# Kernel optimization log

Hardware: AMD Instinct MI355X
Metric: run time of the kernel (lower is better)

The kernel has to match this reference:

```python
import jax, jax.numpy as jnp
import numpy as np

L = 128          # lifted_dim
NS = 50000       # source nodes
NT = 50000       # target nodes
E = 640000       # edges
SLOPE = 0.01     # cfg.leaky_slope (torch LeakyReLU default)
EPS = 1e-5       # BatchNorm eps


def _glorot(key, shape):
    fan_in, fan_out = shape[0], shape[1]
    lim = np.sqrt(6.0 / (fan_in + fan_out)).astype(np.float32)
    return jax.random.uniform(key, shape, jnp.float32, -lim, lim)


def setup_inputs() -> dict:
    key = jax.random.key(0)
    ks = jax.random.split(key, 16)
    x_s = jax.random.normal(ks[0], (NS, L), jnp.float32)
    x_t = jax.random.normal(ks[1], (NT, L), jnp.float32)
    edge_index = jax.random.randint(ks[2], (2, E), 0, NT, jnp.int64)
    edge_attr = jax.random.normal(ks[3], (E, L), jnp.float32)
    x_u = jax.random.normal(ks[4], (L,), jnp.float32)
    M = 2 * L  # message_dim
    U = 4 * L  # update_dim
    params = {
        'W1': _glorot(ks[5], (M, M)), 'b1': jnp.zeros((M,), jnp.float32),
        'W2': _glorot(ks[6], (M, M)), 'b2': jnp.zeros((M,), jnp.float32),
        'U1': _glorot(ks[7], (U, U)), 'c1': jnp.zeros((U,), jnp.float32),
        'U2': _glorot(ks[8], (U, L)), 'c2': jnp.zeros((L,), jnp.float32),
        'gamma': jnp.ones((L,), jnp.float32), 'beta': jnp.zeros((L,), jnp.float32),
    }
    return dict(x_s=x_s, x_t=x_t, edge_index=edge_index, edge_attr=edge_attr, x_u=x_u, **params)


def reference(x_s, x_t, edge_index, edge_attr, x_u,
              W1, b1, W2, b2, U1, c1, U2, c2, gamma, beta):
    src, tgt = edge_index[0], edge_index[1]
    # edge messages: gather source features + edge attrs -> 2-layer MLP
    msg = jnp.concatenate([x_s[src], edge_attr], axis=1)          # [E, 2L]
    msg = jax.nn.leaky_relu(msg @ W1 + b1, negative_slope=SLOPE)
    msg = msg @ W2 + b2                                           # [E, 2L]
    # scatter-add aggregation onto target nodes
    agg = jax.ops.segment_sum(msg, tgt, num_segments=x_t.shape[0])  # [NT, 2L]
    # node update
    xu = jnp.broadcast_to(x_u[None, :], (x_t.shape[0], x_u.shape[0]))
    h = jnp.concatenate([x_t, agg, xu], axis=-1)                  # [NT, 4L]
    h = jax.nn.leaky_relu(h @ U1 + c1, negative_slope=SLOPE)
    h = h @ U2 + c2                                               # [NT, L]
    # BatchNorm1d (training mode: batch statistics, biased variance)
    mu = jnp.mean(h, axis=0)
    var = jnp.var(h, axis=0)
    return gamma * (h - mu) * jax.lax.rsqrt(var + EPS) + beta
```

## Files before the change

kernel.cpp:

```cpp
#include <hip/hip_runtime.h>

typedef unsigned int u32;
typedef unsigned short u16;
typedef __attribute__((ext_vector_type(8))) short short8;
typedef __attribute__((ext_vector_type(8))) unsigned short ushort8v;
typedef __attribute__((ext_vector_type(4))) unsigned short ushort4v;
typedef __attribute__((ext_vector_type(4))) float f32x4;

#define NSRC 50000
#define NTGT 50000
#define NEDGE 640000
#define LDIM 128
#define SLOPE 0.01f

#define MFMA(a, b, c) __builtin_amdgcn_mfma_f32_16x16x32_bf16((a), (b), (c), 0, 0, 0)

__device__ __forceinline__ u16 f2bf(float f) {
  union { float f; u32 u; } v; v.f = f;
  u32 r = v.u + 0x7FFFu + ((v.u >> 16) & 1u);
  return (u16)(r >> 16);
}
__device__ __forceinline__ float bf2f(u16 h) {
  union { u32 u; float f; } v; v.u = ((u32)h) << 16; return v.f;
}

__global__ void k_w2b(const float* __restrict__ W2, const float* __restrict__ U1,
                      float* __restrict__ w2b) {
  const int i = blockIdx.x;
  const int j = threadIdx.x;
  const float* __restrict__ u = U1 + (size_t)128 * 512;
  float a0 = 0.f, a1 = 0.f;
#pragma unroll 8
  for (int k = 0; k < 256; ++k) {
    float w = W2[(size_t)i * 256 + k];
    a0 += w * u[(size_t)k * 512 + j];
    a1 += w * u[(size_t)k * 512 + j + 256];
  }
  w2b[(size_t)i * 512 + j] = a0;
  w2b[(size_t)i * 512 + j + 256] = a1;
}

__global__ void k_bias(const float* __restrict__ U1, const float* __restrict__ xu,
                       const float* __restrict__ b2, const float* __restrict__ c1,
                       float* __restrict__ c1e, float* __restrict__ vb) {
  const int j = threadIdx.x;
  float s = c1[j];
#pragma unroll 4
  for (int k = 0; k < 128; ++k) s += xu[k] * U1[(size_t)(384 + k) * 512 + j];
  float v = 0.f;
#pragma unroll 4
  for (int k = 0; k < 256; ++k) v += b2[k] * U1[(size_t)(128 + k) * 512 + j];
  c1e[j] = s;
  vb[j] = v;
}

__global__ void k_prep(const float* __restrict__ W1, const float* __restrict__ U1,
                       const float* __restrict__ U2, const float* __restrict__ w2b,
                       u16* __restrict__ w1a, u16* __restrict__ w1b,
                       u16* __restrict__ u1e, u16* __restrict__ u2p) {
  int id = blockIdx.x * 256 + threadIdx.x;
  int lane = id & 63, quad = (lane >> 4), l16 = lane & 15;
  if (id < 4096) {
    int g = id >> 6;
    int kc = g >> 4, cb = g & 15;
    const float* s = W1 + (size_t)(kc * 32 + quad * 8) * 256 + cb * 16 + l16;
    ushort8v p;
#pragma unroll
    for (int j = 0; j < 8; ++j) p[j] = f2bf(s[(size_t)j * 256]);
    *(ushort8v*)(w1a + ((size_t)g * 64 + lane) * 8) = p;
  } else if (id < 8192) {
    int g = (id - 4096) >> 6;
    int kc = g >> 4, cb = g & 15;
    const float* s = W1 + (size_t)(128 + kc * 32 + quad * 8) * 256 + cb * 16 + l16;
    ushort8v p;
#pragma unroll
    for (int j = 0; j < 8; ++j) p[j] = f2bf(s[(size_t)j * 256]);
    *(ushort8v*)(w1b + ((size_t)g * 64 + lane) * 8) = p;
  } else if (id < 32768) {
    int g = (id - 8192) >> 6;
    int kc = g >> 5, cb = g & 31;
    int col = cb * 16 + l16;
    ushort8v p;
#pragma unroll
    for (int j = 0; j < 8; ++j) {
      int row = kc * 32 + quad * 8 + j;
      float v = (row < 128) ? U1[(size_t)row * 512 + col]
                            : w2b[(size_t)(row - 128) * 512 + col];
      p[j] = f2bf(v);
    }
    *(ushort8v*)(u1e + ((size_t)g * 64 + lane) * 8) = p;
  } else if (id < 40960) {
    int g = (id - 32768) >> 6;
    int kc = g >> 3, cb = g & 7;
    const float* s = U2 + (size_t)(kc * 32 + quad * 8) * 128 + cb * 16 + l16;
    ushort8v p;
#pragma unroll
    for (int j = 0; j < 8; ++j) p[j] = f2bf(s[(size_t)j * 128]);
    *(ushort8v*)(u2p + ((size_t)g * 64 + lane) * 8) = p;
  }
}

__global__ void k_count(const int* __restrict__ tgt, int* __restrict__ cnt,
                        int* __restrict__ rank) {
  int e = blockIdx.x * 256 + threadIdx.x;
  if (e < NEDGE) rank[e] = atomicAdd(&cnt[tgt[e]], 1);
}

__global__ void k_scan(const int* __restrict__ cnt, int* __restrict__ rowstart) {
  __shared__ int part[1024];
  int tid = threadIdx.x;
  int base = tid * 49;
  int s = 0;
  for (int i = 0; i < 49; ++i) { int idx = base + i; if (idx < NTGT) s += cnt[idx]; }
  part[tid] = s;
  __syncthreads();
  for (int off = 1; off < 1024; off <<= 1) {
    int v = (tid >= off) ? part[tid - off] : 0;
    __syncthreads();
    part[tid] += v;
    __syncthreads();
  }
  int run = (tid > 0) ? part[tid - 1] : 0;
  for (int i = 0; i < 49; ++i) {
    int idx = base + i;
    if (idx < NTGT) { rowstart[idx] = run; run += cnt[idx]; }
  }
  if (tid == 1023) rowstart[NTGT] = part[1023];
}

__global__ void k_pos(const int* __restrict__ tgt, const int* __restrict__ rowstart,
                      int* __restrict__ pos) {
  int e = blockIdx.x * 256 + threadIdx.x;
  if (e < NEDGE) pos[e] = rowstart[tgt[e]] + pos[e];
}

__global__ void k_inv(const int* __restrict__ pos, int* __restrict__ order) {
  int e = blockIdx.x * 256 + threadIdx.x;
  if (e < NEDGE) order[pos[e]] = e;
}

__global__ __launch_bounds__(256, 3) void k_pgemm(
    const float* __restrict__ xs, const u16* __restrict__ w1ap,
    const float* __restrict__ b1, u16* __restrict__ P) {
  __shared__ u16 At[64][136];
  __shared__ u16 Ot[64][264];
  const int tid = threadIdx.x;
  const int base = blockIdx.x * 64;
  {
    const int et = tid >> 2, p = tid & 3;
    const int row = base + et;
    u16* dst = &At[et][p * 32];
    if (row < NSRC) {
      const float4* f4 = (const float4*)(xs + (size_t)row * LDIM + p * 32);
#pragma unroll
      for (int i = 0; i < 4; ++i) {
        float4 a = f4[2 * i], b = f4[2 * i + 1];
        ushort8v pk = { f2bf(a.x), f2bf(a.y), f2bf(a.z), f2bf(a.w),
                        f2bf(b.x), f2bf(b.y), f2bf(b.z), f2bf(b.w) };
        *(ushort8v*)(dst + i * 8) = pk;
      }
    } else {
      ushort8v z = {0, 0, 0, 0, 0, 0, 0, 0};
#pragma unroll
      for (int i = 0; i < 4; ++i) *(ushort8v*)(dst + i * 8) = z;
    }
  }
  __syncthreads();

  const int lane = tid & 63, wid = tid >> 6;
  const int quad = lane >> 4, l16 = lane & 15;
  const int colb = wid * 64;
  const short8* __restrict__ wf = (const short8*)w1ap;

  f32x4 acc[4][4];
#pragma unroll
  for (int a = 0; a < 4; ++a)
#pragma unroll
    for (int b = 0; b < 4; ++b) acc[a][b] = (f32x4){0.f, 0.f, 0.f, 0.f};
#pragma unroll
  for (int kc = 0; kc < 4; ++kc) {
    short8 af[4], bfr[4];
#pragma unroll
    for (int ct = 0; ct < 4; ++ct)
      bfr[ct] = wf[(size_t)(kc * 16 + wid * 4 + ct) * 64 + lane];
#pragma unroll
    for (int rt = 0; rt < 4; ++rt)
      af[rt] = *(const short8*)&At[rt * 16 + l16][kc * 32 + quad * 8];
#pragma unroll
    for (int rt = 0; rt < 4; ++rt)
#pragma unroll
      for (int ct = 0; ct < 4; ++ct)
        acc[rt][ct] = MFMA(af[rt], bfr[ct], acc[rt][ct]);
  }
#pragma unroll
  for (int ct = 0; ct < 4; ++ct) {
    int col = colb + ct * 16 + l16;
    float bias = b1[col];
#pragma unroll
    for (int rt = 0; rt < 4; ++rt)
#pragma unroll
      for (int r = 0; r < 4; ++r) {
        int row = rt * 16 + quad * 4 + r;
        Ot[row][col] = f2bf(acc[rt][ct][r] + bias);
      }
  }
  __syncthreads();
  {
    const int et = tid >> 2, p = tid & 3;
    const int row = base + et;
    if (row < NSRC) {
      u16* dst = P + (size_t)row * 256 + p * 64;
      const u16* sl = &Ot[et][p * 64];
#pragma unroll
      for (int i = 0; i < 8; ++i)
        *(ushort8v*)(dst + i * 8) = *(const ushort8v*)(sl + i * 8);
    }
  }
}

__global__ __launch_bounds__(256, 3) void k_edge(
    const float* __restrict__ ea, const int* __restrict__ srcp,
    const int* __restrict__ tgtp, const int* __restrict__ order,
    const u16* __restrict__ Pg, const u16* __restrict__ w1bp,
    float* __restrict__ agg) {
  __shared__ u16 At[64][136];
  __shared__ u16 Pt[64][264];
  __shared__ int s_tgt[64];
  const int tid = threadIdx.x;
  const int base = blockIdx.x * 64;

  {
    const int et = tid >> 2, p = tid & 3;
    const int e = order[base + et];
    if (p == 0) s_tgt[et] = tgtp[e];
    if (p < 2) {
      const float4* f4 = (const float4*)(ea + (size_t)e * LDIM + p * 64);
      u16* dst = &At[et][p * 64];
#pragma unroll
      for (int i = 0; i < 8; ++i) {
        float4 a = f4[2 * i], b = f4[2 * i + 1];
        ushort8v pk = { f2bf(a.x), f2bf(a.y), f2bf(a.z), f2bf(a.w),
                        f2bf(b.x), f2bf(b.y), f2bf(b.z), f2bf(b.w) };
        *(ushort8v*)(dst + i * 8) = pk;
      }
    } else {
      int sidx = srcp[e];
      const ushort8v* pr = (const ushort8v*)(Pg + (size_t)sidx * 256 + (p - 2) * 128);
      u16* dst = &Pt[et][(p - 2) * 128];
#pragma unroll
      for (int i = 0; i < 16; ++i) *(ushort8v*)(dst + i * 8) = pr[i];
    }
  }
  __syncthreads();

  const int lane = tid & 63, wid = tid >> 6;
  const int quad = lane >> 4, l16 = lane & 15;
  const int colb = wid * 64;
  const short8* __restrict__ wf = (const short8*)w1bp;

  f32x4 acc[4][4];
#pragma unroll
  for (int a = 0; a < 4; ++a)
#pragma unroll
    for (int b = 0; b < 4; ++b) acc[a][b] = (f32x4){0.f, 0.f, 0.f, 0.f};
#pragma unroll
  for (int kc = 0; kc < 4; ++kc) {
    short8 af[4], bfr[4];
#pragma unroll
    for (int ct = 0; ct < 4; ++ct)
      bfr[ct] = wf[(size_t)(kc * 16 + wid * 4 + ct) * 64 + lane];
#pragma unroll
    for (int rt = 0; rt < 4; ++rt)
      af[rt] = *(const short8*)&At[rt * 16 + l16][kc * 32 + quad * 8];
#pragma unroll
    for (int rt = 0; rt < 4; ++rt)
#pragma unroll
      for (int ct = 0; ct < 4; ++ct)
        acc[rt][ct] = MFMA(af[rt], bfr[ct], acc[rt][ct]);
  }
#pragma unroll
  for (int ct = 0; ct < 4; ++ct) {
    int col = colb + ct * 16 + l16;
#pragma unroll
    for (int rt = 0; rt < 4; ++rt)
#pragma unroll
      for (int r = 0; r < 4; ++r) {
        int row = rt * 16 + quad * 4 + r;
        float v = acc[rt][ct][r] + bf2f(Pt[row][col]);
        v = v > 0.f ? v : SLOPE * v;
        Pt[row][col] = f2bf(v);
      }
  }
  __syncthreads();

  {
    const int col = tid;
    float accv = 0.f;
    int prev = s_tgt[0];
    int segstart = 0;
    for (int r = 0; r < 64; ++r) {
      int t = s_tgt[r];
      if (t != prev) {
        float* dst = agg + (size_t)prev * 256 + col;
        if (segstart == 0) atomicAdd(dst, accv);
        else *dst = accv;
        accv = 0.f; prev = t; segstart = r;
      }
      accv += bf2f(Pt[r][col]);
    }
    atomicAdd(agg + (size_t)prev * 256 + col, accv);
  }
}

__global__ __launch_bounds__(256, 4) void k_node(
    const float* __restrict__ xt, const float* __restrict__ agg,
    const int* __restrict__ rowstart, const u16* __restrict__ u1e,
    const u16* __restrict__ u2p, const float* __restrict__ c1e,
    const float* __restrict__ vb, const float* __restrict__ c2,
    float* __restrict__ h2, float* __restrict__ stats) {
  __shared__ u16 ain[32][520];
  __shared__ float sdeg[32];
  const int tid = threadIdx.x;
  const int lane = tid & 63, wid = tid >> 6;
  const int quad = lane >> 4, l16 = lane & 15;
  const int tbase = blockIdx.x * 32;

  for (int s = wid; s < 32; s += 4) {
    int t = tbase + s;
    if (t < NTGT) {
      if (lane < 32) {
        float4 v = ((const float4*)(xt + (size_t)t * LDIM))[lane];
        ushort4v p = { f2bf(v.x), f2bf(v.y), f2bf(v.z), f2bf(v.w) };
        *(ushort4v*)&ain[s][lane * 4] = p;
      }
      if (lane == 0) sdeg[s] = (float)(rowstart[t + 1] - rowstart[t]);
      float4 v = ((const float4*)(agg + (size_t)t * 256))[lane];
      ushort4v p = { f2bf(v.x), f2bf(v.y), f2bf(v.z), f2bf(v.w) };
      *(ushort4v*)&ain[s][128 + lane * 4] = p;
    } else {
      ushort8v z = {0, 0, 0, 0, 0, 0, 0, 0};
      *(ushort8v*)&ain[s][lane * 8] = z;
      if (lane == 0) sdeg[s] = 0.f;
    }
  }
  __syncthreads();

  const short8* __restrict__ u1f = (const short8*)u1e;
  const short8* __restrict__ u2f = (const short8*)u2p;

  f32x4 acc[2][2][4];
#pragma unroll
  for (int h = 0; h < 2; ++h)
#pragma unroll
    for (int a = 0; a < 2; ++a)
#pragma unroll
      for (int b = 0; b < 4; ++b) acc[h][a][b] = (f32x4){0.f, 0.f, 0.f, 0.f};

#pragma unroll 2
  for (int kc = 0; kc < 12; ++kc) {
    short8 af[2];
#pragma unroll
    for (int rt = 0; rt < 2; ++rt)
      af[rt] = *(const short8*)&ain[rt * 16 + l16][kc * 32 + quad * 8];
#pragma unroll
    for (int h = 0; h < 2; ++h) {
      short8 bfr[4];
#pragma unroll
      for (int ct = 0; ct < 4; ++ct)
        bfr[ct] = u1f[(size_t)(kc * 32 + h * 16 + wid * 4 + ct) * 64 + lane];
#pragma unroll
      for (int rt = 0; rt < 2; ++rt)
#pragma unroll
        for (int ct = 0; ct < 4; ++ct)
          acc[h][rt][ct] = MFMA(af[rt], bfr[ct], acc[h][rt][ct]);
    }
  }
  __syncthreads();
#pragma unroll
  for (int h = 0; h < 2; ++h)
#pragma unroll
    for (int ct = 0; ct < 4; ++ct) {
      int col = h * 256 + wid * 64 + ct * 16 + l16;
      float cb = c1e[col], vbb = vb[col];
#pragma unroll
      for (int rt = 0; rt < 2; ++rt)
#pragma unroll
        for (int r = 0; r < 4; ++r) {
          int row = rt * 16 + quad * 4 + r;
          float v = acc[h][rt][ct][r] + cb + sdeg[row] * vbb;
          v = v > 0.f ? v : SLOPE * v;
          ain[row][col] = f2bf(v);
        }
    }
  __syncthreads();

  const int colb2 = wid * 32;
  f32x4 acc2[2][2];
#pragma unroll
  for (int a = 0; a < 2; ++a)
#pragma unroll
    for (int b = 0; b < 2; ++b) acc2[a][b] = (f32x4){0.f, 0.f, 0.f, 0.f};
#pragma unroll 4
  for (int kc = 0; kc < 16; ++kc) {
    short8 af[2], bfr[2];
#pragma unroll
    for (int ct = 0; ct < 2; ++ct)
      bfr[ct] = u2f[(size_t)(kc * 8 + wid * 2 + ct) * 64 + lane];
#pragma unroll
    for (int rt = 0; rt < 2; ++rt)
      af[rt] = *(const short8*)&ain[rt * 16 + l16][kc * 32 + quad * 8];
#pragma unroll
    for (int rt = 0; rt < 2; ++rt)
#pragma unroll
      for (int ct = 0; ct < 2; ++ct)
        acc2[rt][ct] = MFMA(af[rt], bfr[ct], acc2[rt][ct]);
  }
  float s1[2] = {0.f, 0.f}, s2[2] = {0.f, 0.f};
#pragma unroll
  for (int ct = 0; ct < 2; ++ct) {
    int col = colb2 + ct * 16 + l16;
    float cb = c2[col];
#pragma unroll
    for (int rt = 0; rt < 2; ++rt)
#pragma unroll
      for (int r = 0; r < 4; ++r) {
        int row = rt * 16 + quad * 4 + r;
        int t = tbase + row;
        if (t < NTGT) {
          float v = acc2[rt][ct][r] + cb;
          h2[(size_t)t * LDIM + col] = v;
          s1[ct] += v; s2[ct] += v * v;
        }
      }
  }
#pragma unroll
  for (int ct = 0; ct < 2; ++ct) {
    float a = s1[ct], b = s2[ct];
    a += __shfl_down(a, 32); b += __shfl_down(b, 32);
    a += __shfl_down(a, 16); b += __shfl_down(b, 16);
    if (lane < 16) {
      atomicAdd(&stats[colb2 + ct * 16 + l16], a);
      atomicAdd(&stats[128 + colb2 + ct * 16 + l16], b);
    }
  }
}

__global__ void k_bnfin(const float* __restrict__ stats, const float* __restrict__ gamma,
                        const float* __restrict__ beta, float* __restrict__ ss) {
  int c = threadIdx.x;
  if (c < 128) {
    float mu = stats[c] * (1.0f / NTGT);
    float var = stats[128 + c] * (1.0f / NTGT) - mu * mu;
    float rs = rsqrtf(var + 1e-5f);
    float sc = gamma[c] * rs;
    ss[c] = sc;
    ss[128 + c] = beta[c] - mu * sc;
  }
}

__global__ void k_bnapply(const float* __restrict__ h2, const float* __restrict__ ss,
                          float* __restrict__ out) {
  int i = blockIdx.x * 256 + threadIdx.x;
  const int total = NTGT * LDIM / 4;
  const float4* h4 = (const float4*)h2;
  const float4* sc4 = (const float4*)ss;
  const float4* sh4 = (const float4*)(ss + 128);
  float4* o4 = (float4*)out;
  for (; i < total; i += gridDim.x * 256) {
    int cg = i & 31;
    float4 h = h4[i], sc = sc4[cg], sh = sh4[cg];
    float4 r = { h.x * sc.x + sh.x, h.y * sc.y + sh.y,
                 h.z * sc.z + sh.z, h.w * sc.w + sh.w };
    o4[i] = r;
  }
}

extern "C" void kernel_launch(void* const* d_in, const int* in_sizes, int n_in,
                              void* d_out, int out_size, void* d_ws, size_t ws_size,
                              hipStream_t stream) {
  (void)in_sizes; (void)n_in; (void)out_size; (void)ws_size;
  const float* xs    = (const float*)d_in[0];
  const float* xt    = (const float*)d_in[1];
  const int*   ei    = (const int*)d_in[2];
  const float* ea    = (const float*)d_in[3];
  const float* xu    = (const float*)d_in[4];
  const float* W1    = (const float*)d_in[5];
  const float* b1    = (const float*)d_in[6];
  const float* W2    = (const float*)d_in[7];
  const float* b2    = (const float*)d_in[8];
  const float* U1    = (const float*)d_in[9];
  const float* c1    = (const float*)d_in[10];
  const float* U2    = (const float*)d_in[11];
  const float* c2    = (const float*)d_in[12];
  const float* gamma = (const float*)d_in[13];
  const float* beta  = (const float*)d_in[14];

  char* ws = (char*)d_ws;
  u16* w1a   = (u16*)(ws + 0x000000);
  u16* w1b   = (u16*)(ws + 0x010000);
  u16* u1e   = (u16*)(ws + 0x020000);
  u16* u2p   = (u16*)(ws + 0x080000);
  float* w2b = (float*)(ws + 0x0A0000);
  float* c1e = (float*)(ws + 0x120000);
  float* vbv = (float*)(ws + 0x120800);
  int* cnt   = (int*)(ws + 0x130000);
  int* rowst = (int*)(ws + 0x161000);
  int* pos   = (int*)(ws + 0x192000);
  float* stats = (float*)(ws + 0x404000);
  float* ss    = stats + 256;
  int* order = (int*)(ws + 0x405000);
  float* agg = (float*)(ws + 0x680000);
  u16*   Pbuf = (u16*)(ws + 0x3760000);
  float* h2   = (float*)(ws + 0x3760000);

  const int* srcp = ei;
  const int* tgtp = ei + NEDGE;

  hipMemsetAsync(cnt, 0, NTGT * 4, stream);
  hipMemsetAsync(stats, 0, 256 * 4, stream);
  hipMemsetAsync(agg, 0, (size_t)NTGT * 256 * 4, stream);
  k_w2b<<<256, 256, 0, stream>>>(W2, U1, w2b);
  k_bias<<<1, 512, 0, stream>>>(U1, xu, b2, c1, c1e, vbv);
  k_prep<<<160, 256, 0, stream>>>(W1, U1, U2, w2b, w1a, w1b, u1e, u2p);
  k_count<<<2500, 256, 0, stream>>>(tgtp, cnt, pos);
  k_scan<<<1, 1024, 0, stream>>>(cnt, rowst);
  k_pos<<<2500, 256, 0, stream>>>(tgtp, rowst, pos);
  k_inv<<<2500, 256, 0, stream>>>(pos, order);
  k_pgemm<<<782, 256, 0, stream>>>(xs, w1a, b1, Pbuf);
  k_edge<<<10000, 256, 0, stream>>>(ea, srcp, tgtp, order, Pbuf, w1b, agg);
  k_node<<<1563, 256, 0, stream>>>(xt, agg, rowst, u1e, u2p, c1e, vbv, c2, h2, stats);
  k_bnfin<<<1, 128, 0, stream>>>(stats, gamma, beta, ss);
  k_bnapply<<<6250, 256, 0, stream>>>(h2, ss, (float*)d_out);
}
```

Before: 905.1 us.

## Load edge attrs directly into MFMA fragments, drop LDS staging, fuse pos/inv

The edge kernel no longer stages edge_attr through a shared-memory tile. Each lane loads its fp32 fragment from global memory and converts it to bf16 in registers right before the MFMA. This removes an LDS buffer and a barrier and allows higher occupancy (launch bounds 4). Segment boundaries are precomputed as a wavefront ballot mask, and the position and inverse-permutation kernels are merged into one launch. The risk is less coalesced global loads for the edge attributes.

New measurement: 984.9 us. +8.8%, slower.

```diff
diff --git a/kernel.cpp b/kernel.cpp
--- a/kernel.cpp
+++ b/kernel.cpp
@@ -128,15 +128,10 @@
   if (tid == 1023) rowstart[NTGT] = part[1023];
 }
 
-__global__ void k_pos(const int* __restrict__ tgt, const int* __restrict__ rowstart,
-                      int* __restrict__ pos) {
+__global__ void k_posinv(const int* __restrict__ tgt, const int* __restrict__ rowstart,
+                         const int* __restrict__ rank, int* __restrict__ order) {
   int e = blockIdx.x * 256 + threadIdx.x;
-  if (e < NEDGE) pos[e] = rowstart[tgt[e]] + pos[e];
-}
-
-__global__ void k_inv(const int* __restrict__ pos, int* __restrict__ order) {
-  int e = blockIdx.x * 256 + threadIdx.x;
-  if (e < NEDGE) order[pos[e]] = e;
+  if (e < NEDGE) order[rowstart[tgt[e]] + rank[e]] = e;
 }
 
 __global__ __launch_bounds__(256, 3) void k_pgemm(
@@ -218,14 +213,14 @@
   }
 }
 
-__global__ __launch_bounds__(256, 3) void k_edge(
+__global__ __launch_bounds__(256, 4) void k_edge(
     const float* __restrict__ ea, const int* __restrict__ srcp,
     const int* __restrict__ tgtp, const int* __restrict__ order,
     const u16* __restrict__ Pg, const u16* __restrict__ w1bp,
     float* __restrict__ agg) {
-  __shared__ u16 At[64][136];
   __shared__ u16 Pt[64][264];
   __shared__ int s_tgt[64];
+  __shared__ unsigned long long s_mask;
   const int tid = threadIdx.x;
   const int base = blockIdx.x * 64;
 
@@ -233,51 +228,59 @@
     const int et = tid >> 2, p = tid & 3;
     const int e = order[base + et];
     if (p == 0) s_tgt[et] = tgtp[e];
-    if (p < 2) {
-      const float4* f4 = (const float4*)(ea + (size_t)e * LDIM + p * 64);
-      u16* dst = &At[et][p * 64];
-#pragma unroll
-      for (int i = 0; i < 8; ++i) {
-        float4 a = f4[2 * i], b = f4[2 * i + 1];
-        ushort8v pk = { f2bf(a.x), f2bf(a.y), f2bf(a.z), f2bf(a.w),
-                        f2bf(b.x), f2bf(b.y), f2bf(b.z), f2bf(b.w) };
-        *(ushort8v*)(dst + i * 8) = pk;
-      }
-    } else {
-      int sidx = srcp[e];
-      const ushort8v* pr = (const ushort8v*)(Pg + (size_t)sidx * 256 + (p - 2) * 128);
-      u16* dst = &Pt[et][(p - 2) * 128];
-#pragma unroll
-      for (int i = 0; i < 16; ++i) *(ushort8v*)(dst + i * 8) = pr[i];
-    }
-  }
-  __syncthreads();
+    const int sidx = srcp[e];
+    const ushort8v* pr = (const ushort8v*)(Pg + (size_t)sidx * 256 + p * 64);
+    u16* dst = &Pt[et][p * 64];
+#pragma unroll
+    for (int i = 0; i < 8; ++i) *(ushort8v*)(dst + i * 8) = pr[i];
+  }
+  if (tid < 64) {
+    int tcur = tgtp[order[base + tid]];
+    int tprv = (tid > 0) ? tgtp[order[base + tid - 1]] : tcur;
+    unsigned long long m = __ballot(tcur != tprv);
+    if (tid == 0) s_mask = m;
+  }
 
   const int lane = tid & 63, wid = tid >> 6;
   const int quad = lane >> 4, l16 = lane & 15;
   const int colb = wid * 64;
   const short8* __restrict__ wf = (const short8*)w1bp;
 
+  const float* ab[4];
+#pragma unroll
+  for (int rt = 0; rt < 4; ++rt)
+    ab[rt] = ea + (size_t)order[base + rt * 16 + l16] * LDIM + quad * 8;
+
   f32x4 acc[4][4];
 #pragma unroll
   for (int a = 0; a < 4; ++a)
 #pragma unroll
     for (int b = 0; b < 4; ++b) acc[a][b] = (f32x4){0.f, 0.f, 0.f, 0.f};
+
 #pragma unroll
   for (int kc = 0; kc < 4; ++kc) {
-    short8 af[4], bfr[4];
+    short8 af[4];
+#pragma unroll
+    for (int rt = 0; rt < 4; ++rt) {
+      f32x4 x = *(const f32x4*)(ab[rt] + kc * 32);
+      f32x4 y = *(const f32x4*)(ab[rt] + kc * 32 + 4);
+      af[rt] = (short8){ (short)f2bf(x[0]), (short)f2bf(x[1]),
+                         (short)f2bf(x[2]), (short)f2bf(x[3]),
+                         (short)f2bf(y[0]), (short)f2bf(y[1]),
+                         (short)f2bf(y[2]), (short)f2bf(y[3]) };
+    }
+    short8 bfr[4];
 #pragma unroll
     for (int ct = 0; ct < 4; ++ct)
       bfr[ct] = wf[(size_t)(kc * 16 + wid * 4 + ct) * 64 + lane];
 #pragma unroll
     for (int rt = 0; rt < 4; ++rt)
-      af[rt] = *(const short8*)&At[rt * 16 + l16][kc * 32 + quad * 8];
-#pragma unroll
-    for (int rt = 0; rt < 4; ++rt)
 #pragma unroll
       for (int ct = 0; ct < 4; ++ct)
         acc[rt][ct] = MFMA(af[rt], bfr[ct], acc[rt][ct]);
   }
+  __syncthreads();
+
 #pragma unroll
   for (int ct = 0; ct < 4; ++ct) {
     int col = colb + ct * 16 + l16;
@@ -294,21 +297,20 @@
   __syncthreads();
 
   {
+    const unsigned long long mask = s_mask;
     const int col = tid;
     float accv = 0.f;
-    int prev = s_tgt[0];
     int segstart = 0;
     for (int r = 0; r < 64; ++r) {
-      int t = s_tgt[r];
-      if (t != prev) {
-        float* dst = agg + (size_t)prev * 256 + col;
+      if ((mask >> r) & 1ull) {
+        float* dst = agg + (size_t)s_tgt[r - 1] * 256 + col;
         if (segstart == 0) atomicAdd(dst, accv);
         else *dst = accv;
-        accv = 0.f; prev = t; segstart = r;
+        accv = 0.f; segstart = r;
       }
       accv += bf2f(Pt[r][col]);
     }
-    atomicAdd(agg + (size_t)prev * 256 + col, accv);
+    atomicAdd(agg + (size_t)s_tgt[63] * 256 + col, accv);
   }
 }
 
@@ -505,7 +507,7 @@
   float* vbv = (float*)(ws + 0x120800);
   int* cnt   = (int*)(ws + 0x130000);
   int* rowst = (int*)(ws + 0x161000);
-  int* pos   = (int*)(ws + 0x192000);
+  int* rank  = (int*)(ws + 0x192000);
   float* stats = (float*)(ws + 0x404000);
   float* ss    = stats + 256;
   int* order = (int*)(ws + 0x405000);
@@ -522,10 +524,9 @@
   k_w2b<<<256, 256, 0, stream>>>(W2, U1, w2b);
   k_bias<<<1, 512, 0, stream>>>(U1, xu, b2, c1, c1e, vbv);
   k_prep<<<160, 256, 0, stream>>>(W1, U1, U2, w2b, w1a, w1b, u1e, u2p);
-  k_count<<<2500, 256, 0, stream>>>(tgtp, cnt, pos);
+  k_count<<<2500, 256, 0, stream>>>(tgtp, cnt, rank);
   k_scan<<<1, 1024, 0, stream>>>(cnt, rowst);
-  k_pos<<<2500, 256, 0, stream>>>(tgtp, rowst, pos);
-  k_inv<<<2500, 256, 0, stream>>>(pos, order);
+  k_posinv<<<2500, 256, 0, stream>>>(tgtp, rowst, rank, order);
   k_pgemm<<<782, 256, 0, stream>>>(xs, w1a, b1, Pbuf);
   k_edge<<<10000, 256, 0, stream>>>(ea, srcp, tgtp, order, Pbuf, w1b, agg);
   k_node<<<1563, 256, 0, stream>>>(xt, agg, rowst, u1e, u2p, c1e, vbv, c2, h2, stats);
```
